# Performance work log

Hardware: AMD Instinct MI355X
Metric: run time of the kernel (lower is better)

The kernel has to match this reference:

```python
import jax, jax.numpy as jnp
import numpy as np

EPS = 1e-06


def setup_inputs() -> dict:
    key = jax.random.key(0)
    k1, k2 = jax.random.split(key)
    x = jax.random.normal(k1, (256, 4096), dtype=jnp.float32)
    # learned parameter, init matches torch.randn(...) * 0.1
    shapelets = jax.random.normal(k2, (8, 16, 128), dtype=jnp.float32) * 0.1
    return {"x": x, "shapelets": shapelets}


def reference(x, shapelets):
    B, T = x.shape
    C, Kc, L = shapelets.shape
    nwin = T - L + 1  # stride-1 unfold

    # sliding windows: [B, nwin, L] (same materialization as torch unfold)
    idx = jnp.arange(nwin)[:, None] + jnp.arange(L)[None, :]
    x_win = x[:, idx]

    # z-normalize each window (population std, unbiased=False)
    mu_x = jnp.mean(x_win, axis=2, keepdims=True)
    var_x = jnp.mean((x_win - mu_x) ** 2, axis=2, keepdims=True)
    std_x = jnp.sqrt(var_x) + EPS
    x_norm = (x_win - mu_x) / std_x

    # z-normalize shapelets per class/shapelet
    mu_s = jnp.mean(shapelets, axis=2, keepdims=True)
    var_s = jnp.mean((shapelets - mu_s) ** 2, axis=2, keepdims=True)
    std_s = jnp.sqrt(var_s) + EPS
    s_norm = (shapelets - mu_s) / std_s

    # normalized cross-correlation: [B, nwin, C, Kc]
    corr = jnp.einsum('btl,ckl->btck', x_norm, s_norm) / L

    # max over window positions, concat classes -> [B, C*Kc]
    max_vals = jnp.max(corr, axis=1)  # [B, C, Kc]
    return max_vals.reshape(B, C * Kc)
```

## Files before the change

### kernel.cpp

```cpp
#include <hip/hip_runtime.h>
#include <hip/hip_bf16.h>

typedef __attribute__((ext_vector_type(8))) short short8;
typedef __attribute__((ext_vector_type(4))) float float4v;

#define T_LEN 4096
#define L_LEN 128
#define NWIN  3969
#define CK    128

__device__ __forceinline__ unsigned short f2bf(float f) {
    unsigned u = __float_as_uint(f);
    u += 0x7fffu + ((u >> 16) & 1u);
    return (unsigned short)(u >> 16);
}

__global__ void prep_sh(const float* __restrict__ sh,
                        unsigned short* __restrict__ wsB) {
    const int ck = blockIdx.x;
    const int l  = threadIdx.x;
    __shared__ float rs[2], rq[2];
    const int lane = l & 63, wv = l >> 6;

    float v = sh[ck * L_LEN + l];
    float s = v, q = v * v;
    #pragma unroll
    for (int off = 32; off >= 1; off >>= 1) {
        s += __shfl_xor(s, off);
        q += __shfl_xor(q, off);
    }
    if (lane == 0) { rs[wv] = s; rq[wv] = q; }
    __syncthreads();
    float sm = rs[0] + rs[1], sq = rq[0] + rq[1];
    float mu  = sm * (1.f / L_LEN);
    float var = fmaxf(sq * (1.f / L_LEN) - mu * mu, 0.f);
    float inv = 1.f / (sqrtf(var) + 1e-6f);
    unsigned short b = f2bf((v - mu) * inv);
    const int nt = ck >> 4, n = ck & 15;
    const int kt = l >> 5, qd = (l >> 3) & 3, jj = l & 7;
    wsB[((((nt * 4 + kt) * 64) + qd * 16 + n) << 3) + jj] = b;
}

__global__ __launch_bounds__(512, 2)
void conv_row(const float* __restrict__ x,
              const unsigned short* __restrict__ wsB,
              float* __restrict__ out) {
    __shared__ alignas(16) unsigned short xb[8][T_LEN];
    __shared__ float sty[T_LEN];
    __shared__ float PSs[513], PQs[513];
    __shared__ float grpS[8], grpQ[8];
    __shared__ float wmax[8][CK];

    const int tid  = threadIdx.x;
    const int lane = tid & 63;
    const int wv   = tid >> 6;
    const int row  = blockIdx.x;
    const float4* xr4 = (const float4*)(x + row * T_LEN);

    short8 Bf[8][4];
    {
        const short8* Bp = (const short8*)wsB;
        #pragma unroll
        for (int nt = 0; nt < 8; ++nt)
            #pragma unroll
            for (int kt = 0; kt < 4; ++kt)
                Bf[nt][kt] = Bp[(nt * 4 + kt) * 64 + lane];
    }

    float v[16];
    {
        float4 a0 = xr4[2 * tid];
        float4 a1 = xr4[2 * tid + 1];
        float4 a2 = make_float4(0.f, 0.f, 0.f, 0.f), a3 = a2;
        if (tid < 511) { a2 = xr4[2 * tid + 2]; a3 = xr4[2 * tid + 3]; }
        v[0]=a0.x; v[1]=a0.y; v[2]=a0.z;  v[3]=a0.w;
        v[4]=a1.x; v[5]=a1.y; v[6]=a1.z;  v[7]=a1.w;
        v[8]=a2.x; v[9]=a2.y; v[10]=a2.z; v[11]=a2.w;
        v[12]=a3.x; v[13]=a3.y; v[14]=a3.z; v[15]=a3.w;
    }
    unsigned short bb[16];
    #pragma unroll
    for (int i = 0; i < 16; ++i) bb[i] = f2bf(v[i]);
    #pragma unroll
    for (int c = 0; c < 8; ++c) {
        short8 w8;
        #pragma unroll
        for (int j = 0; j < 8; ++j) w8[j] = (short)bb[c + j];
        *(short8*)&xb[c][8 * tid] = w8;
    }

    float s = 0.f, q = 0.f;
    #pragma unroll
    for (int i = 0; i < 8; ++i) { s += v[i]; q += v[i] * v[i]; }
    float is = s, iq = q;
    #pragma unroll
    for (int off = 1; off < 64; off <<= 1) {
        float ts = __shfl_up(is, off);
        float tq = __shfl_up(iq, off);
        if (lane >= off) { is += ts; iq += tq; }
    }
    if (lane == 63) { grpS[wv] = is; grpQ[wv] = iq; }
    __syncthreads();
    float os = 0.f, oq = 0.f;
    #pragma unroll
    for (int w = 0; w < 7; ++w) if (w < wv) { os += grpS[w]; oq += grpQ[w]; }
    PSs[tid] = os + is - s;
    PQs[tid] = oq + iq - q;
    if (tid == 511) { PSs[512] = os + is; PQs[512] = oq + iq; }
    __syncthreads();

    if (tid < 497) {
        float S = PSs[tid + 16] - PSs[tid];
        float Q = PQs[tid + 16] - PQs[tid];
        float4 b0 = make_float4(0.f, 0.f, 0.f, 0.f), b1 = b0;
        if (tid <= 495) { b0 = xr4[2 * tid + 32]; b1 = xr4[2 * tid + 33]; }
        float xn[8] = {b0.x, b0.y, b0.z, b0.w, b1.x, b1.y, b1.z, b1.w};
        #pragma unroll
        for (int e = 0; e < 8; ++e) {
            int w = 8 * tid + e;
            if (w < NWIN) {
                float mu  = S * (1.f / L_LEN);
                float var = fmaxf(Q * (1.f / L_LEN) - mu * mu, 0.f);
                float sd  = sqrtf(var) + 1e-6f;
                sty[w] = 1.f / (sd * (float)L_LEN);
                S += xn[e] - v[e];
                Q += xn[e] * xn[e] - v[e] * v[e];
            }
        }
    }
    __syncthreads();

    const int abase = (lane & 15) + (lane >> 4);
    const int q4    = (lane >> 4) * 4;
    float vmax[8];
    #pragma unroll
    for (int nt = 0; nt < 8; ++nt) vmax[nt] = -1e30f;

    #pragma unroll 1
    for (int ii = 0; ii < 32; ++ii) {
        const int ci = (ii + 4 * wv) & 31;
        const int T0 = (ci < 31) ? ci * 128 : (NWIN - 128);
        const int e0 = T0 + wv;
        const int c  = e0 & 7;
        const int b8 = e0 >> 3;

        float sr[4];
        #pragma unroll
        for (int r = 0; r < 4; ++r) sr[r] = sty[e0 + 8 * (q4 + r)];
        short8 af[4];
        #pragma unroll
        for (int kt = 0; kt < 4; ++kt)
            af[kt] = *(const short8*)&xb[c][8 * (b8 + abase + 4 * kt)];

        float4v acc[8];
        #pragma unroll
        for (int nt = 0; nt < 8; ++nt) acc[nt] = float4v{0.f, 0.f, 0.f, 0.f};

        #pragma unroll
        for (int kt = 0; kt < 4; ++kt)
            #pragma unroll
            for (int nt = 0; nt < 8; ++nt)
                acc[nt] = __builtin_amdgcn_mfma_f32_16x16x32_bf16(
                    af[kt], Bf[nt][kt], acc[nt], 0, 0, 0);

        #pragma unroll
        for (int nt = 0; nt < 8; ++nt) {
            float m01 = fmaxf(acc[nt][0] * sr[0], acc[nt][1] * sr[1]);
            float m23 = fmaxf(acc[nt][2] * sr[2], acc[nt][3] * sr[3]);
            vmax[nt] = fmaxf(vmax[nt], fmaxf(m01, m23));
        }
    }

    #pragma unroll
    for (int nt = 0; nt < 8; ++nt) {
        float vx = vmax[nt];
        vx = fmaxf(vx, __shfl_xor(vx, 16));
        vx = fmaxf(vx, __shfl_xor(vx, 32));
        if (lane < 16) wmax[wv][nt * 16 + lane] = vx;
    }
    __syncthreads();
    if (tid < CK) {
        float m = wmax[0][tid];
        #pragma unroll
        for (int w = 1; w < 8; ++w) m = fmaxf(m, wmax[w][tid]);
        out[row * CK + tid] = m;
    }
}

extern "C" void kernel_launch(void* const* d_in, const int* in_sizes, int n_in,
                              void* d_out, int out_size, void* d_ws, size_t ws_size,
                              hipStream_t stream) {
    (void)in_sizes; (void)n_in; (void)out_size; (void)ws_size;
    const float* x  = (const float*)d_in[0];
    const float* sh = (const float*)d_in[1];
    unsigned short* wsB = (unsigned short*)d_ws;
    float* out = (float*)d_out;

    prep_sh<<<128, 128, 0, stream>>>(sh, wsB);
    conv_row<<<256, 512, 0, stream>>>(x, wsB, out);
}
```

Before: 81.99 us.

## Switch correlation MFMA from 16x16x32 to 32x32x16 tiles

Reorganizes the shapelet operand layout and the main correlation loop to use 32x32x16 bf16 MFMA instructions. Each wave now handles 256 window positions per iteration, split into two halves of 64 shapelets, with 16-element accumulators. A-fragments are loaded per k-step inside the loop. s_setprio is raised around the MFMA bursts. The aim is fewer A-operand LDS reads per FLOP and higher MFMA efficiency. The cost is larger accumulator register usage and a different tail-window overlap scheme.

```diff
diff --git a/kernel.cpp b/kernel.cpp
--- a/kernel.cpp
+++ b/kernel.cpp
@@ -2,7 +2,7 @@
 #include <hip/hip_bf16.h>
 
 typedef __attribute__((ext_vector_type(8))) short short8;
-typedef __attribute__((ext_vector_type(4))) float float4v;
+typedef __attribute__((ext_vector_type(16))) float f32x16;
 
 #define T_LEN 4096
 #define L_LEN 128
@@ -36,9 +36,9 @@
     float var = fmaxf(sq * (1.f / L_LEN) - mu * mu, 0.f);
     float inv = 1.f / (sqrtf(var) + 1e-6f);
     unsigned short b = f2bf((v - mu) * inv);
-    const int nt = ck >> 4, n = ck & 15;
-    const int kt = l >> 5, qd = (l >> 3) & 3, jj = l & 7;
-    wsB[((((nt * 4 + kt) * 64) + qd * 16 + n) << 3) + jj] = b;
+    const int nt = ck >> 5, n = ck & 31;
+    const int kt = l >> 4, hi = (l >> 3) & 1, j = l & 7;
+    wsB[((((nt * 8 + kt) * 64) + hi * 32 + n) << 3) + j] = b;
 }
 
 __global__ __launch_bounds__(512, 2)
@@ -57,14 +57,14 @@
     const int row  = blockIdx.x;
     const float4* xr4 = (const float4*)(x + row * T_LEN);
 
-    short8 Bf[8][4];
+    short8 Bf[4][8];
     {
         const short8* Bp = (const short8*)wsB;
         #pragma unroll
-        for (int nt = 0; nt < 8; ++nt)
-            #pragma unroll
-            for (int kt = 0; kt < 4; ++kt)
-                Bf[nt][kt] = Bp[(nt * 4 + kt) * 64 + lane];
+        for (int nt = 0; nt < 4; ++nt)
+            #pragma unroll
+            for (int kt = 0; kt < 8; ++kt)
+                Bf[nt][kt] = Bp[(nt * 8 + kt) * 64 + lane];
     }
 
     float v[16];
@@ -130,53 +130,58 @@
     }
     __syncthreads();
 
-    const int abase = (lane & 15) + (lane >> 4);
-    const int q4    = (lane >> 4) * 4;
-    float vmax[8];
-    #pragma unroll
-    for (int nt = 0; nt < 8; ++nt) vmax[nt] = -1e30f;
+    const int hi  = lane >> 5;
+    const int m32 = lane & 31;
+    float vmax[4];
+    #pragma unroll
+    for (int nt = 0; nt < 4; ++nt) vmax[nt] = -1e30f;
 
     #pragma unroll 1
-    for (int ii = 0; ii < 32; ++ii) {
-        const int ci = (ii + 4 * wv) & 31;
-        const int T0 = (ci < 31) ? ci * 128 : (NWIN - 128);
+    for (int ii = 0; ii < 16; ++ii) {
+        const int ci = (ii + 2 * wv) & 15;
+        const int T0 = (ci < 15) ? ci * 256 : (NWIN - 256);
         const int e0 = T0 + wv;
         const int c  = e0 & 7;
-        const int b8 = e0 >> 3;
-
-        float sr[4];
-        #pragma unroll
-        for (int r = 0; r < 4; ++r) sr[r] = sty[e0 + 8 * (q4 + r)];
-        short8 af[4];
-        #pragma unroll
-        for (int kt = 0; kt < 4; ++kt)
-            af[kt] = *(const short8*)&xb[c][8 * (b8 + abase + 4 * kt)];
-
-        float4v acc[8];
-        #pragma unroll
-        for (int nt = 0; nt < 8; ++nt) acc[nt] = float4v{0.f, 0.f, 0.f, 0.f};
-
-        #pragma unroll
-        for (int kt = 0; kt < 4; ++kt)
-            #pragma unroll
-            for (int nt = 0; nt < 8; ++nt)
-                acc[nt] = __builtin_amdgcn_mfma_f32_16x16x32_bf16(
-                    af[kt], Bf[nt][kt], acc[nt], 0, 0, 0);
-
-        #pragma unroll
-        for (int nt = 0; nt < 8; ++nt) {
-            float m01 = fmaxf(acc[nt][0] * sr[0], acc[nt][1] * sr[1]);
-            float m23 = fmaxf(acc[nt][2] * sr[2], acc[nt][3] * sr[3]);
-            vmax[nt] = fmaxf(vmax[nt], fmaxf(m01, m23));
+        const int B0 = e0 >> 3;
+
+        float sr[16];
+        #pragma unroll
+        for (int r = 0; r < 16; ++r)
+            sr[r] = sty[e0 + 32 * hi + 8 * (r & 3) + 64 * (r >> 2)];
+
+        const unsigned short* ab = &xb[c][8 * (B0 + m32 + hi)];
+
+        #pragma unroll
+        for (int h = 0; h < 2; ++h) {
+            f32x16 a0, a1;
+            #pragma unroll
+            for (int r = 0; r < 16; ++r) { a0[r] = 0.f; a1[r] = 0.f; }
+
+            __builtin_amdgcn_s_setprio(1);
+            #pragma unroll
+            for (int kt = 0; kt < 8; ++kt) {
+                short8 af = *(const short8*)(ab + 16 * kt);
+                a0 = __builtin_amdgcn_mfma_f32_32x32x16_bf16(
+                    af, Bf[2 * h][kt], a0, 0, 0, 0);
+                a1 = __builtin_amdgcn_mfma_f32_32x32x16_bf16(
+                    af, Bf[2 * h + 1][kt], a1, 0, 0, 0);
+            }
+            __builtin_amdgcn_s_setprio(0);
+
+            float v0 = vmax[2 * h], v1 = vmax[2 * h + 1];
+            #pragma unroll
+            for (int r = 0; r < 16; ++r) {
+                v0 = fmaxf(v0, a0[r] * sr[r]);
+                v1 = fmaxf(v1, a1[r] * sr[r]);
+            }
+            vmax[2 * h] = v0; vmax[2 * h + 1] = v1;
         }
     }
 
     #pragma unroll
-    for (int nt = 0; nt < 8; ++nt) {
-        float vx = vmax[nt];
-        vx = fmaxf(vx, __shfl_xor(vx, 16));
-        vx = fmaxf(vx, __shfl_xor(vx, 32));
-        if (lane < 16) wmax[wv][nt * 16 + lane] = vx;
+    for (int nt = 0; nt < 4; ++nt) {
+        float vx = fmaxf(vmax[nt], __shfl_xor(vmax[nt], 32));
+        if (lane < 32) wmax[wv][nt * 32 + m32] = vx;
     }
     __syncthreads();
     if (tid < CK) {
```

New measurement: 85.76 us. 1.05x slower.
